# Kernel tuning notes

Measured on AMD Instinct MI355X. Metric: run time of the kernel, lower is better.

## Reference

```python
import jax, jax.numpy as jnp
import numpy as np

B, T, C, H = 4, 2048, 2048, 16
D = C // H  # head dim = 128


def setup_inputs() -> dict:
    key = jax.random.key(0)
    k1, k2, k3, k4 = jax.random.split(key, 4)
    x = jax.random.normal(k1, (B, T, C), dtype=jnp.float32)
    # per-token key mask; force token 0 valid so no causal row is fully masked
    tok_mask = jax.random.randint(k2, (B, T), 0, 2).astype(bool).at[:, 0].set(True)
    s = 1.0 / np.sqrt(C).astype(np.float32)
    W_qkv = jax.random.normal(k3, (C, 3 * C), dtype=jnp.float32) * s
    W_proj = jax.random.normal(k4, (C, C), dtype=jnp.float32) * s
    return {"x": x, "tok_mask": tok_mask, "W_qkv": W_qkv, "W_proj": W_proj}


def reference(x, tok_mask, W_qkv, W_proj):
    Bx, Tx, Cx = x.shape
    qkv = x @ W_qkv                              # [B,T,3C]
    q, k, v = jnp.split(qkv, 3, axis=-1)
    q = q.reshape(Bx, Tx, H, D)
    k = k.reshape(Bx, Tx, H, D)
    v = v.reshape(Bx, Tx, H, D)
    scale = 1.0 / np.sqrt(D).astype(np.float32)
    scores = jnp.einsum('bqhd,bkhd->bhqk', q, k) * scale  # [B,H,T,T]
    causal = jnp.tril(jnp.ones((Tx, Tx), dtype=bool))      # [T,T]
    # tok_mask broadcasts over the query dim (key mask), AND-ed with causal
    mask = tok_mask[:, None, :] & causal                   # [B,T,T]
    scores = jnp.where(mask[:, None, :, :], scores, -jnp.inf)
    attn = jax.nn.softmax(scores, axis=-1)                 # dropout p=0 -> identity
    y = jnp.einsum('bhqk,bkhd->bqhd', attn, v).reshape(Bx, Tx, Cx)
    return y @ W_proj
```

## Files before the change

### kernel.cpp

```cpp
#include <hip/hip_runtime.h>
#include <hip/hip_bf16.h>
#include <stdint.h>

typedef __bf16 bf16;
typedef __bf16 bf16x8 __attribute__((ext_vector_type(8)));
typedef float f32x4 __attribute__((ext_vector_type(4)));
typedef unsigned short u16;
typedef unsigned int u32;

constexpr int NB = 4;
constexpr int NT = 2048;
constexpr int NC = 2048;
constexpr int NH = 16;
constexpr int ND = 128;
constexpr int NC3 = 6144;

__device__ __forceinline__ void gload16(const void* g, void* l) {
  __builtin_amdgcn_global_load_lds((const __attribute__((address_space(1))) void*)g,
                                   (__attribute__((address_space(3))) void*)l, 16, 0, 0);
}

__device__ __forceinline__ u32 pack_bf16(float a, float b) {
  return (u32)__builtin_bit_cast(u16, (bf16)a) | ((u32)__builtin_bit_cast(u16, (bf16)b) << 16);
}

__global__ __launch_bounds__(256) void ingest_k(const float* __restrict__ raw, bf16* __restrict__ out, long n) {
  long i = ((long)blockIdx.x * 256 + threadIdx.x) * 8;
  if (i >= n) return;
  f32x4 a = *(const f32x4*)(raw + i), b = *(const f32x4*)(raw + i + 4);
  bf16x8 o;
  o[0] = (bf16)a[0]; o[1] = (bf16)a[1]; o[2] = (bf16)a[2]; o[3] = (bf16)a[3];
  o[4] = (bf16)b[0]; o[5] = (bf16)b[1]; o[6] = (bf16)b[2]; o[7] = (bf16)b[3];
  *(bf16x8*)(out + i) = o;
}

__global__ void mask_prep_k(const void* raw, int* out) {
  __shared__ int s_gt1, s_oddnz, s_allb, s_allf, s_allh;
  if (threadIdx.x == 0) { s_gt1 = 0; s_oddnz = 0; s_allb = 1; s_allf = 1; s_allh = 1; }
  __syncthreads();
  const unsigned int* mw = (const unsigned int*)raw;
  int gt1 = 0, oddnz = 0, allb = 1, allf = 1, allh = 1;
  for (int i = threadIdx.x; i < 2048; i += 256) {
    unsigned v = mw[i];
    if (v > 1u) gt1 = 1;
    if ((i & 1) && v) oddnz = 1;
#pragma unroll
    for (int bb = 0; bb < 4; ++bb) { unsigned by = (v >> (8*bb)) & 0xffu; if (by > 1u) allb = 0; }
    if (v != 0u && v != 0x3F800000u) allf = 0;
    unsigned lo = v & 0xffffu, hi = v >> 16;
    if ((lo != 0u && lo != 0x3F80u) || (hi != 0u && hi != 0x3F80u)) allh = 0;
  }
  if (gt1) atomicOr(&s_gt1, 1);
  if (oddnz) atomicOr(&s_oddnz, 1);
  if (!allb) atomicAnd(&s_allb, 0);
  if (!allf) atomicAnd(&s_allf, 0);
  if (!allh) atomicAnd(&s_allh, 0);
  __syncthreads();
  int mode;
  if (!s_gt1)       mode = s_oddnz ? 0 : 2;
  else if (s_allf)  mode = 3;
  else if (s_allb)  mode = 1;
  else if (s_allh)  mode = 4;
  else              mode = 0;
  for (int i = threadIdx.x; i < NB*NT; i += 256) {
    int v;
    if (mode == 0)      v = (((const int*)raw)[i] != 0);
    else if (mode == 1) v = (((const unsigned char*)raw)[i] != 0);
    else if (mode == 2) v = (((const long long*)raw)[i] != 0);
    else if (mode == 3) v = (((const unsigned int*)raw)[i] != 0);
    else                v = (((const unsigned short*)raw)[i] != 0);
    out[i] = v;
  }
}

__global__ __launch_bounds__(256) void transpose_f32_k(const float* __restrict__ in, bf16* __restrict__ out,
                                                       int in_rs, int out_rs) {
  __shared__ __align__(16) bf16 t[64][72];
  const int r0 = blockIdx.y << 6, c0 = blockIdx.x << 6;
  const int tid = threadIdx.x;
#pragma unroll
  for (int i = 0; i < 4; ++i) {
    int slot = i*256 + tid, row = slot >> 4, c4 = slot & 15;
    f32x4 v = *(const f32x4*)(in + (long)(r0 + row)*in_rs + c0 + c4*4);
#pragma unroll
    for (int e = 0; e < 4; ++e) t[c4*4 + e][row] = (bf16)v[e];
  }
  __syncthreads();
#pragma unroll
  for (int i = 0; i < 2; ++i) {
    int slot = i*256 + tid, row = slot >> 3, c8 = slot & 7;
    bf16x8 v = *(const bf16x8*)(&t[row][c8*8]);
    *(bf16x8*)(out + (long)(c0 + row)*out_rs + r0 + c8*8) = v;
  }
}

__global__ __launch_bounds__(256) void vtrans_k(const bf16* __restrict__ qkv, bf16* __restrict__ vt) {
  __shared__ __align__(16) bf16 t[64][72];
  const int tt = blockIdx.x, dh = blockIdx.y, bh = blockIdx.z;
  const int b = bh >> 4, h = bh & 15;
  const int tid = threadIdx.x;
  const bf16* src = qkv + (long)(b*NT + tt*64)*NC3 + (2*NC + h*ND + dh*64);
#pragma unroll
  for (int i = 0; i < 2; ++i) {
    int slot = i*256 + tid, row = slot >> 3, c8 = slot & 7;
    bf16x8 v = *(const bf16x8*)(src + (long)row*NC3 + c8*8);
#pragma unroll
    for (int e = 0; e < 8; ++e) t[c8*8 + e][row] = v[e];
  }
  __syncthreads();
  bf16* dst = vt + ((long)bh*ND + dh*64)*NT + tt*64;
#pragma unroll
  for (int i = 0; i < 2; ++i) {
    int slot = i*256 + tid, row = slot >> 3, c8 = slot & 7;
    bf16x8 v = *(const bf16x8*)(&t[row][c8*8]);
    *(bf16x8*)(dst + (long)row*NT + c8*8) = v;
  }
}

template <typename OT>
__global__ __launch_bounds__(512, 2) void gemm256_k(const bf16* __restrict__ A, const bf16* __restrict__ BT,
                                                    OT* __restrict__ Cout, int M, int N, int K, int nbx) {
  const int nwg = gridDim.x;
  const int bid = blockIdx.x;
  const int cpx = nwg >> 3;
  const int swz = (bid & 7) * cpx + (bid >> 3);
  const int bx = swz % nbx, by = swz / nbx;
  const long m0 = (long)by << 8, n0 = (long)bx << 8;

  const int tid = threadIdx.x, w = tid >> 6, l = tid & 63, g = l >> 4, r = l & 15;
  const int wm = w >> 2, wn = w & 3;

  __shared__ __align__(16) char As[2][32768];
  __shared__ __align__(16) char Bs[2][32768];

  long aoff[4], boff[4];
  int slo[4];
#pragma unroll
  for (int i = 0; i < 4; ++i) {
    int s = i*512 + tid, row = s >> 3, c = s & 7, cp = c ^ (row & 7);
    aoff[i] = (m0 + row)*(long)K + cp*8;
    boff[i] = (n0 + row)*(long)K + cp*8;
    slo[i] = (i*512 + w*64) << 4;
  }

  const f32x4 z4 = {0.f, 0.f, 0.f, 0.f};
  f32x4 acc[8][4];
#pragma unroll
  for (int i = 0; i < 8; ++i)
#pragma unroll
    for (int j = 0; j < 4; ++j) acc[i][j] = z4;

  const int nk = K >> 6;
#pragma unroll
  for (int i = 0; i < 4; ++i) {
    gload16(A + aoff[i], As[0] + slo[i]);
    gload16(BT + boff[i], Bs[0] + slo[i]);
  }
  __syncthreads();

  bf16x8 af[8], bfr[4];

  for (int t = 0; t < nk; ++t) {
    const int cur = t & 1;
    const char* Ac = As[cur];
    const char* Bc = Bs[cur];

#pragma unroll
    for (int mi = 0; mi < 4; ++mi)
#pragma unroll
      for (int kk = 0; kk < 2; ++kk) {
        int row = wm*128 + mi*16 + r;
        af[mi*2+kk] = *(const bf16x8*)(Ac + row*128 + (((kk*4 + g) ^ (row & 7)) << 4));
      }
#pragma unroll
    for (int ni = 0; ni < 2; ++ni)
#pragma unroll
      for (int kk = 0; kk < 2; ++kk) {
        int row = wn*64 + ni*16 + r;
        bfr[ni*2+kk] = *(const bf16x8*)(Bc + row*128 + (((kk*4 + g) ^ (row & 7)) << 4));
      }
    if (t + 1 < nk) {
      const long ko = (long)(t+1) << 6;
#pragma unroll
      for (int i = 0; i < 4; ++i) {
        gload16(A + aoff[i] + ko, As[cur^1] + slo[i]);
        gload16(BT + boff[i] + ko, Bs[cur^1] + slo[i]);
      }
    }
    __builtin_amdgcn_s_setprio(1);
#pragma unroll
    for (int mi = 0; mi < 4; ++mi)
#pragma unroll
      for (int ni = 0; ni < 2; ++ni)
#pragma unroll
        for (int kk = 0; kk < 2; ++kk)
          acc[mi][ni] = __builtin_amdgcn_mfma_f32_16x16x32_bf16(af[mi*2+kk], bfr[ni*2+kk], acc[mi][ni], 0, 0, 0);
    __builtin_amdgcn_s_setprio(0);
    __builtin_amdgcn_s_barrier();

#pragma unroll
    for (int mi = 0; mi < 4; ++mi)
#pragma unroll
      for (int kk = 0; kk < 2; ++kk) {
        int row = wm*128 + 64 + mi*16 + r;
        af[mi*2+kk] = *(const bf16x8*)(Ac + row*128 + (((kk*4 + g) ^ (row & 7)) << 4));
      }
    __builtin_amdgcn_s_setprio(1);
#pragma unroll
    for (int mi = 0; mi < 4; ++mi)
#pragma unroll
      for (int ni = 0; ni < 2; ++ni)
#pragma unroll
        for (int kk = 0; kk < 2; ++kk)
          acc[4+mi][ni] = __builtin_amdgcn_mfma_f32_16x16x32_bf16(af[mi*2+kk], bfr[ni*2+kk], acc[4+mi][ni], 0, 0, 0);
    __builtin_amdgcn_s_setprio(0);
    __builtin_amdgcn_s_barrier();

#pragma unroll
    for (int ni = 0; ni < 2; ++ni)
#pragma unroll
      for (int kk = 0; kk < 2; ++kk) {
        int row = wn*64 + 32 + ni*16 + r;
        bfr[ni*2+kk] = *(const bf16x8*)(Bc + row*128 + (((kk*4 + g) ^ (row & 7)) << 4));
      }
    __builtin_amdgcn_s_setprio(1);
#pragma unroll
    for (int mi = 0; mi < 4; ++mi)
#pragma unroll
      for (int ni = 0; ni < 2; ++ni)
#pragma unroll
        for (int kk = 0; kk < 2; ++kk)
          acc[4+mi][2+ni] = __builtin_amdgcn_mfma_f32_16x16x32_bf16(af[mi*2+kk], bfr[ni*2+kk], acc[4+mi][2+ni], 0, 0, 0);
    __builtin_amdgcn_s_setprio(0);
    __builtin_amdgcn_s_barrier();

#pragma unroll
    for (int mi = 0; mi < 4; ++mi)
#pragma unroll
      for (int kk = 0; kk < 2; ++kk) {
        int row = wm*128 + mi*16 + r;
        af[mi*2+kk] = *(const bf16x8*)(Ac + row*128 + (((kk*4 + g) ^ (row & 7)) << 4));
      }
    __builtin_amdgcn_s_setprio(1);
#pragma unroll
    for (int mi = 0; mi < 4; ++mi)
#pragma unroll
      for (int ni = 0; ni < 2; ++ni)
#pragma unroll
        for (int kk = 0; kk < 2; ++kk)
          acc[mi][2+ni] = __builtin_amdgcn_mfma_f32_16x16x32_bf16(af[mi*2+kk], bfr[ni*2+kk], acc[mi][2+ni], 0, 0, 0);
    __builtin_amdgcn_s_setprio(0);
    __syncthreads();
  }

#pragma unroll
  for (int mi = 0; mi < 8; ++mi)
#pragma unroll
    for (int ni = 0; ni < 4; ++ni)
#pragma unroll
      for (int j = 0; j < 4; ++j) {
        long mr = m0 + wm*128 + mi*16 + 4*g + j;
        long nc = n0 + wn*64 + ni*16 + r;
        Cout[mr*(long)N + nc] = (OT)acc[mi][ni][j];
      }
}

__global__ __launch_bounds__(256, 2) void attn_k(const bf16* __restrict__ qkv, const bf16* __restrict__ vt,
                                                 const int* __restrict__ mask, bf16* __restrict__ y) {
  const int qx = blockIdx.x, h = blockIdx.y, b = blockIdx.z;
  const int qt = (qx & 1) ? (31 - (qx >> 1)) : (qx >> 1);
  const int tid = threadIdx.x, w = tid >> 6, l = tid & 63, g = l >> 4, r = l & 15;
  const int q0 = qt << 6;
  const int bh = b*NH + h;
  const int ntiles = qt + 1;
  const int qrow = q0 + w*16 + r;

  __shared__ __align__(16) char Klds[2][16384];
  __shared__ __align__(16) char Vlds[2][16384];
  __shared__ __align__(16) char Plds[8192];
  __shared__ char Mc[2048];
  char* Pl = Plds + (w << 11);

  for (int i = tid; i < q0 + 64; i += 256) Mc[i] = (char)(mask[b*NT + i] != 0);

  long koff[4], voff[4];
  int klo[4];
#pragma unroll
  for (int i = 0; i < 4; ++i) {
    int slot = i*256 + tid;
    int row = slot >> 4, c = slot & 15, cp = c ^ (row & 7);
    koff[i] = (long)row*NC3 + cp*8;
    klo[i] = (i*256 + w*64) << 4;
    int vrow = slot >> 3, vc = slot & 7, vcp = vc ^ (vrow & 7);
    voff[i] = (long)vrow*NT + vcp*8;
  }
  const bf16* kbase0 = qkv + (long)(b*NT)*NC3 + (NC + h*ND);
  const bf16* vbase0 = vt + (long)bh*ND*NT;

  bf16x8 qf[4];
  {
    const bf16* qp = qkv + (long)(b*NT + qrow)*NC3 + h*ND + g*8;
#pragma unroll
    for (int dk = 0; dk < 4; ++dk) qf[dk] = *(const bf16x8*)(qp + dk*32);
  }

  const f32x4 z4 = {0.f, 0.f, 0.f, 0.f};
  f32x4 acc[8];
#pragma unroll
  for (int i = 0; i < 8; ++i) acc[i] = z4;
  float m_run = 0.0f;
  float l_run = 0.0f;

  const float SCL = 0.08838834764831845f * 1.4426950408889634f;

#pragma unroll
  for (int i = 0; i < 4; ++i) {
    gload16(kbase0 + koff[i], Klds[0] + klo[i]);
    gload16(vbase0 + voff[i], Vlds[0] + klo[i]);
  }
  __syncthreads();

  for (int kt = 0; kt < ntiles; ++kt) {
    const int cur = kt & 1;
    if (kt + 1 < ntiles) {
      const bf16* kb = kbase0 + (long)((kt+1)*64)*NC3;
      const bf16* vb = vbase0 + (kt+1)*64;
#pragma unroll
      for (int i = 0; i < 4; ++i) {
        gload16(kb + koff[i], Klds[cur^1] + klo[i]);
        gload16(vb + voff[i], Vlds[cur^1] + klo[i]);
      }
    }
    const char* Kl = Klds[cur];
    const char* Vl = Vlds[cur];
    const int key0 = kt*64;
    const bool act = (key0 <= q0 + w*16 + 15);

    if (act) {
      u32 mw_[4];
#pragma unroll
      for (int kc = 0; kc < 4; ++kc) mw_[kc] = *(const u32*)(Mc + key0 + kc*16 + 4*g);

      float tv[4][4];
      __builtin_amdgcn_s_setprio(1);
#pragma unroll
      for (int kc = 0; kc < 4; ++kc) {
        const int krow = kc*16 + r;
        f32x4 s = z4;
#pragma unroll
        for (int dk = 0; dk < 4; ++dk) {
          bf16x8 kf = *(const bf16x8*)(Kl + krow*256 + (((dk*4 + g) ^ (krow & 7)) << 4));
          s = __builtin_amdgcn_mfma_f32_16x16x32_bf16(kf, qf[dk], s, 0, 0, 0);
        }
#pragma unroll
        for (int j = 0; j < 4; ++j) {
          const int key = key0 + kc*16 + 4*g + j;
          const bool ok = ((mw_[kc] >> (8*j)) & 0xffu) && (key <= qrow);
          tv[kc][j] = ok ? s[j]*SCL : -3.0e38f;
        }
      }
      __builtin_amdgcn_s_setprio(0);

      float tmax = -3.0e38f;
#pragma unroll
      for (int kc = 0; kc < 4; ++kc)
#pragma unroll
        for (int j = 0; j < 4; ++j) tmax = fmaxf(tmax, tv[kc][j]);
      tmax = fmaxf(tmax, __shfl_xor(tmax, 16));
      tmax = fmaxf(tmax, __shfl_xor(tmax, 32));

      if (!__all(tmax <= m_run + 8.0f)) {
        float mn = fmaxf(m_run, tmax);
        float al = exp2f(m_run - mn);
        m_run = mn;
        l_run *= al;
        float alj[4];
#pragma unroll
        for (int j = 0; j < 4; ++j) alj[j] = __shfl(al, 4*g + j);
#pragma unroll
        for (int d0 = 0; d0 < 8; ++d0)
#pragma unroll
          for (int j = 0; j < 4; ++j) acc[d0][j] *= alj[j];
      }

      float rs = 0.f;
      u32 pk0[4], pk1[4];
#pragma unroll
      for (int kc = 0; kc < 4; ++kc) {
        float p0 = exp2f(tv[kc][0] - m_run), p1 = exp2f(tv[kc][1] - m_run);
        float p2 = exp2f(tv[kc][2] - m_run), p3 = exp2f(tv[kc][3] - m_run);
        rs += (p0 + p1) + (p2 + p3);
        pk0[kc] = pack_bf16(p0, p1);
        pk1[kc] = pack_bf16(p2, p3);
      }
      rs += __shfl_xor(rs, 16);
      rs += __shfl_xor(rs, 32);
      l_run += rs;
#pragma unroll
      for (int kc = 0; kc < 4; ++kc) {
        const int off = (kc*32 + g*8) ^ ((r & 7) << 4);
        uint2 wv; wv.x = pk0[kc]; wv.y = pk1[kc];
        *(uint2*)(Pl + r*128 + off) = wv;
      }
      asm volatile("s_waitcnt lgkmcnt(0)" ::: "memory");
      __builtin_amdgcn_sched_barrier(0);
      bf16x8 pa[2];
#pragma unroll
      for (int kk = 0; kk < 2; ++kk)
        pa[kk] = *(const bf16x8*)(Pl + r*128 + ((kk*64 + g*16) ^ ((r & 7) << 4)));

      __builtin_amdgcn_s_setprio(1);
#pragma unroll
      for (int d0 = 0; d0 < 8; ++d0) {
        const int vrow = d0*16 + r;
#pragma unroll
        for (int kk = 0; kk < 2; ++kk) {
          bf16x8 vf = *(const bf16x8*)(Vl + vrow*128 + (((kk*4 + g) ^ (vrow & 7)) << 4));
          acc[d0] = __builtin_amdgcn_mfma_f32_16x16x32_bf16(pa[kk], vf, acc[d0], 0, 0, 0);
        }
      }
      __builtin_amdgcn_s_setprio(0);
    }
    __syncthreads();
  }

  float lr[4];
#pragma unroll
  for (int j = 0; j < 4; ++j) lr[j] = __shfl(l_run, 4*g + j);
#pragma unroll
  for (int d0 = 0; d0 < 8; ++d0)
#pragma unroll
    for (int j = 0; j < 4; ++j) {
      int qr = q0 + w*16 + 4*g + j;
      y[(long)(b*NT + qr)*NC + h*ND + d0*16 + r] = (bf16)(acc[d0][j] / lr[j]);
    }
}

extern "C" void kernel_launch(void* const* d_in, const int* in_sizes, int n_in,
                              void* d_out, int out_size, void* d_ws, size_t ws_size,
                              hipStream_t stream) {
  const float* xr     = (const float*)d_in[0];
  const void*  tok    = d_in[1];
  const float* wqkvr  = (const float*)d_in[2];
  const float* wprojr = (const float*)d_in[3];
  float* out = (float*)d_out;
  char* ws = (char*)d_ws;

  bf16* qkv    = (bf16*)(ws);
  bf16* yattn  = (bf16*)(ws + 100663296L);
  bf16* wT     = (bf16*)(ws + 134217728L);
  bf16* wpT    = (bf16*)(ws + 159383552L);
  bf16* xb     = (bf16*)(ws + 167772160L);
  bf16* vtb    = xb;
  int*  maskI  = (int*)(ws + 201326592L);

  mask_prep_k<<<1, 256, 0, stream>>>(tok, maskI);
  ingest_k<<<8192, 256, 0, stream>>>(xr, xb, 16777216L);
  transpose_f32_k<<<dim3(96, 32), 256, 0, stream>>>(wqkvr, wT, NC3, NC);
  transpose_f32_k<<<dim3(32, 32), 256, 0, stream>>>(wprojr, wpT, NC, NC);
  gemm256_k<bf16><<<768, 512, 0, stream>>>(xb, wT, qkv, 8192, 6144, 2048, 24);
  vtrans_k<<<dim3(32, 2, 64), 256, 0, stream>>>(qkv, vtb);
  attn_k<<<dim3(32, 16, 4), 256, 0, stream>>>(qkv, vtb, maskI, yattn);
  gemm256_k<float><<<256, 512, 0, stream>>>(yattn, wpT, out, 8192, 2048, 2048, 8);
}
```

Baseline: 589.8 us.

## Double query rows per wave in attention to reuse K/V tiles

The attention kernel now processes 128 query rows per block, with each wave handling two 16-row query groups that share the same K and V fragments loaded from LDS. This halves the grid and the K/V global-to-LDS traffic per query row, and amortises LDS fragment reads over twice the MFMA work. In exchange, register pressure roughly doubles (two accumulator sets), so launch bounds drop to one block per SIMD-occupancy target. The coarser causal tiles also add some wasted work on diagonal blocks and reduce load balancing granularity.

```diff
diff --git a/kernel.cpp b/kernel.cpp
--- a/kernel.cpp
+++ b/kernel.cpp
@@ -265,23 +265,25 @@
       }
 }
 
-__global__ __launch_bounds__(256, 2) void attn_k(const bf16* __restrict__ qkv, const bf16* __restrict__ vt,
+__global__ __launch_bounds__(256, 1) void attn_k(const bf16* __restrict__ qkv, const bf16* __restrict__ vt,
                                                  const int* __restrict__ mask, bf16* __restrict__ y) {
   const int qx = blockIdx.x, h = blockIdx.y, b = blockIdx.z;
-  const int qt = (qx & 1) ? (31 - (qx >> 1)) : (qx >> 1);
+  const int qb = (qx & 1) ? (15 - (qx >> 1)) : (qx >> 1);
   const int tid = threadIdx.x, w = tid >> 6, l = tid & 63, g = l >> 4, r = l & 15;
-  const int q0 = qt << 6;
+  const int q0 = qb << 7;
   const int bh = b*NH + h;
-  const int ntiles = qt + 1;
-  const int qrow = q0 + w*16 + r;
+  const int ntiles = (qb << 1) + 2;
+  const int qrowA = q0 + w*32 + r;
+  const int qrowB = qrowA + 16;
 
   __shared__ __align__(16) char Klds[2][16384];
   __shared__ __align__(16) char Vlds[2][16384];
-  __shared__ __align__(16) char Plds[8192];
+  __shared__ __align__(16) char Plds[16384];
   __shared__ char Mc[2048];
-  char* Pl = Plds + (w << 11);
-
-  for (int i = tid; i < q0 + 64; i += 256) Mc[i] = (char)(mask[b*NT + i] != 0);
+  char* PlA = Plds + (w << 12);
+  char* PlB = PlA + 2048;
+
+  for (int i = tid; i < q0 + 128; i += 256) Mc[i] = (char)(mask[b*NT + i] != 0);
 
   long koff[4], voff[4];
   int klo[4];
@@ -297,19 +299,23 @@
   const bf16* kbase0 = qkv + (long)(b*NT)*NC3 + (NC + h*ND);
   const bf16* vbase0 = vt + (long)bh*ND*NT;
 
-  bf16x8 qf[4];
+  bf16x8 qfA[4], qfB[4];
   {
-    const bf16* qp = qkv + (long)(b*NT + qrow)*NC3 + h*ND + g*8;
-#pragma unroll
-    for (int dk = 0; dk < 4; ++dk) qf[dk] = *(const bf16x8*)(qp + dk*32);
+    const bf16* qpA = qkv + (long)(b*NT + qrowA)*NC3 + h*ND + g*8;
+    const bf16* qpB = qkv + (long)(b*NT + qrowB)*NC3 + h*ND + g*8;
+#pragma unroll
+    for (int dk = 0; dk < 4; ++dk) {
+      qfA[dk] = *(const bf16x8*)(qpA + dk*32);
+      qfB[dk] = *(const bf16x8*)(qpB + dk*32);
+    }
   }
 
   const f32x4 z4 = {0.f, 0.f, 0.f, 0.f};
-  f32x4 acc[8];
-#pragma unroll
-  for (int i = 0; i < 8; ++i) acc[i] = z4;
-  float m_run = 0.0f;
-  float l_run = 0.0f;
+  f32x4 accA[8], accB[8];
+#pragma unroll
+  for (int i = 0; i < 8; ++i) { accA[i] = z4; accB[i] = z4; }
+  float m_runA = 0.0f, l_runA = 0.0f;
+  float m_runB = 0.0f, l_runB = 0.0f;
 
   const float SCL = 0.08838834764831845f * 1.4426950408889634f;
 
@@ -334,80 +340,122 @@
     const char* Kl = Klds[cur];
     const char* Vl = Vlds[cur];
     const int key0 = kt*64;
-    const bool act = (key0 <= q0 + w*16 + 15);
-
-    if (act) {
+    const bool actB = (key0 <= q0 + w*32 + 31);
+    const bool actA = (key0 <= q0 + w*32 + 15);
+
+    if (actB) {
       u32 mw_[4];
 #pragma unroll
       for (int kc = 0; kc < 4; ++kc) mw_[kc] = *(const u32*)(Mc + key0 + kc*16 + 4*g);
 
-      float tv[4][4];
+      float tvA[4][4], tvB[4][4];
       __builtin_amdgcn_s_setprio(1);
 #pragma unroll
       for (int kc = 0; kc < 4; ++kc) {
         const int krow = kc*16 + r;
-        f32x4 s = z4;
-#pragma unroll
-        for (int dk = 0; dk < 4; ++dk) {
-          bf16x8 kf = *(const bf16x8*)(Kl + krow*256 + (((dk*4 + g) ^ (krow & 7)) << 4));
-          s = __builtin_amdgcn_mfma_f32_16x16x32_bf16(kf, qf[dk], s, 0, 0, 0);
+        bf16x8 kf[4];
+#pragma unroll
+        for (int dk = 0; dk < 4; ++dk)
+          kf[dk] = *(const bf16x8*)(Kl + krow*256 + (((dk*4 + g) ^ (krow & 7)) << 4));
+        f32x4 sB = z4;
+#pragma unroll
+        for (int dk = 0; dk < 4; ++dk)
+          sB = __builtin_amdgcn_mfma_f32_16x16x32_bf16(kf[dk], qfB[dk], sB, 0, 0, 0);
+        f32x4 sA = z4;
+        if (actA) {
+#pragma unroll
+          for (int dk = 0; dk < 4; ++dk)
+            sA = __builtin_amdgcn_mfma_f32_16x16x32_bf16(kf[dk], qfA[dk], sA, 0, 0, 0);
         }
 #pragma unroll
         for (int j = 0; j < 4; ++j) {
           const int key = key0 + kc*16 + 4*g + j;
-          const bool ok = ((mw_[kc] >> (8*j)) & 0xffu) && (key <= qrow);
-          tv[kc][j] = ok ? s[j]*SCL : -3.0e38f;
+          const bool km = ((mw_[kc] >> (8*j)) & 0xffu) != 0;
+          tvB[kc][j] = (km && key <= qrowB) ? sB[j]*SCL : -3.0e38f;
+          tvA[kc][j] = (km && key <= qrowA) ? sA[j]*SCL : -3.0e38f;
         }
       }
       __builtin_amdgcn_s_setprio(0);
 
-      float tmax = -3.0e38f;
-#pragma unroll
-      for (int kc = 0; kc < 4; ++kc)
-#pragma unroll
-        for (int j = 0; j < 4; ++j) tmax = fmaxf(tmax, tv[kc][j]);
-      tmax = fmaxf(tmax, __shfl_xor(tmax, 16));
-      tmax = fmaxf(tmax, __shfl_xor(tmax, 32));
-
-      if (!__all(tmax <= m_run + 8.0f)) {
-        float mn = fmaxf(m_run, tmax);
-        float al = exp2f(m_run - mn);
-        m_run = mn;
-        l_run *= al;
-        float alj[4];
-#pragma unroll
-        for (int j = 0; j < 4; ++j) alj[j] = __shfl(al, 4*g + j);
-#pragma unroll
-        for (int d0 = 0; d0 < 8; ++d0)
-#pragma unroll
-          for (int j = 0; j < 4; ++j) acc[d0][j] *= alj[j];
-      }
-
-      float rs = 0.f;
-      u32 pk0[4], pk1[4];
-#pragma unroll
-      for (int kc = 0; kc < 4; ++kc) {
-        float p0 = exp2f(tv[kc][0] - m_run), p1 = exp2f(tv[kc][1] - m_run);
-        float p2 = exp2f(tv[kc][2] - m_run), p3 = exp2f(tv[kc][3] - m_run);
-        rs += (p0 + p1) + (p2 + p3);
-        pk0[kc] = pack_bf16(p0, p1);
-        pk1[kc] = pack_bf16(p2, p3);
-      }
-      rs += __shfl_xor(rs, 16);
-      rs += __shfl_xor(rs, 32);
-      l_run += rs;
-#pragma unroll
-      for (int kc = 0; kc < 4; ++kc) {
-        const int off = (kc*32 + g*8) ^ ((r & 7) << 4);
-        uint2 wv; wv.x = pk0[kc]; wv.y = pk1[kc];
-        *(uint2*)(Pl + r*128 + off) = wv;
-      }
+      {
+        float tmax = -3.0e38f;
+#pragma unroll
+        for (int kc = 0; kc < 4; ++kc)
+#pragma unroll
+          for (int j = 0; j < 4; ++j) tmax = fmaxf(tmax, tvB[kc][j]);
+        tmax = fmaxf(tmax, __shfl_xor(tmax, 16));
+        tmax = fmaxf(tmax, __shfl_xor(tmax, 32));
+        if (!__all(tmax <= m_runB + 8.0f)) {
+          float mn = fmaxf(m_runB, tmax);
+          float al = exp2f(m_runB - mn);
+          m_runB = mn;
+          l_runB *= al;
+          float alj[4];
+#pragma unroll
+          for (int j = 0; j < 4; ++j) alj[j] = __shfl(al, 4*g + j);
+#pragma unroll
+          for (int d0 = 0; d0 < 8; ++d0)
+#pragma unroll
+            for (int j = 0; j < 4; ++j) accB[d0][j] *= alj[j];
+        }
+        float rs = 0.f;
+#pragma unroll
+        for (int kc = 0; kc < 4; ++kc) {
+          float p0 = exp2f(tvB[kc][0] - m_runB), p1 = exp2f(tvB[kc][1] - m_runB);
+          float p2 = exp2f(tvB[kc][2] - m_runB), p3 = exp2f(tvB[kc][3] - m_runB);
+          rs += (p0 + p1) + (p2 + p3);
+          const int off = (kc*32 + g*8) ^ ((r & 7) << 4);
+          uint2 wv; wv.x = pack_bf16(p0, p1); wv.y = pack_bf16(p2, p3);
+          *(uint2*)(PlB + r*128 + off) = wv;
+        }
+        rs += __shfl_xor(rs, 16);
+        rs += __shfl_xor(rs, 32);
+        l_runB += rs;
+      }
+      if (actA) {
+        float tmax = -3.0e38f;
+#pragma unroll
+        for (int kc = 0; kc < 4; ++kc)
+#pragma unroll
+          for (int j = 0; j < 4; ++j) tmax = fmaxf(tmax, tvA[kc][j]);
+        tmax = fmaxf(tmax, __shfl_xor(tmax, 16));
+        tmax = fmaxf(tmax, __shfl_xor(tmax, 32));
+        if (!__all(tmax <= m_runA + 8.0f)) {
+          float mn = fmaxf(m_runA, tmax);
+          float al = exp2f(m_runA - mn);
+          m_runA = mn;
+          l_runA *= al;
+          float alj[4];
+#pragma unroll
+          for (int j = 0; j < 4; ++j) alj[j] = __shfl(al, 4*g + j);
+#pragma unroll
+          for (int d0 = 0; d0 < 8; ++d0)
+#pragma unroll
+            for (int j = 0; j < 4; ++j) accA[d0][j] *= alj[j];
+        }
+        float rs = 0.f;
+#pragma unroll
+        for (int kc = 0; kc < 4; ++kc) {
+          float p0 = exp2f(tvA[kc][0] - m_runA), p1 = exp2f(tvA[kc][1] - m_runA);
+          float p2 = exp2f(tvA[kc][2] - m_runA), p3 = exp2f(tvA[kc][3] - m_runA);
+          rs += (p0 + p1) + (p2 + p3);
+          const int off = (kc*32 + g*8) ^ ((r & 7) << 4);
+          uint2 wv; wv.x = pack_bf16(p0, p1); wv.y = pack_bf16(p2, p3);
+          *(uint2*)(PlA + r*128 + off) = wv;
+        }
+        rs += __shfl_xor(rs, 16);
+        rs += __shfl_xor(rs, 32);
+        l_runA += rs;
+      }
+
       asm volatile("s_waitcnt lgkmcnt(0)" ::: "memory");
       __builtin_amdgcn_sched_barrier(0);
-      bf16x8 pa[2];
-#pragma unroll
-      for (int kk = 0; kk < 2; ++kk)
-        pa[kk] = *(const bf16x8*)(Pl + r*128 + ((kk*64 + g*16) ^ ((r & 7) << 4)));
+      bf16x8 paA[2], paB[2];
+#pragma unroll
+      for (int kk = 0; kk < 2; ++kk) {
+        paB[kk] = *(const bf16x8*)(PlB + r*128 + ((kk*64 + g*16) ^ ((r & 7) << 4)));
+        paA[kk] = *(const bf16x8*)(PlA + r*128 + ((kk*64 + g*16) ^ ((r & 7) << 4)));
+      }
 
       __builtin_amdgcn_s_setprio(1);
 #pragma unroll
@@ -416,7 +464,8 @@
 #pragma unroll
         for (int kk = 0; kk < 2; ++kk) {
           bf16x8 vf = *(const bf16x8*)(Vl + vrow*128 + (((kk*4 + g) ^ (vrow & 7)) << 4));
-          acc[d0] = __builtin_amdgcn_mfma_f32_16x16x32_bf16(pa[kk], vf, acc[d0], 0, 0, 0);
+          accB[d0] = __builtin_amdgcn_mfma_f32_16x16x32_bf16(paB[kk], vf, accB[d0], 0, 0, 0);
+          if (actA) accA[d0] = __builtin_amdgcn_mfma_f32_16x16x32_bf16(paA[kk], vf, accA[d0], 0, 0, 0);
         }
       }
       __builtin_amdgcn_s_setprio(0);
@@ -424,16 +473,22 @@
     __syncthreads();
   }
 
-  float lr[4];
-#pragma unroll
-  for (int j = 0; j < 4; ++j) lr[j] = __shfl(l_run, 4*g + j);
-#pragma unroll
-  for (int d0 = 0; d0 < 8; ++d0)
+  {
+    float lrA[4], lrB[4];
 #pragma unroll
     for (int j = 0; j < 4; ++j) {
-      int qr = q0 + w*16 + 4*g + j;
-      y[(long)(b*NT + qr)*NC + h*ND + d0*16 + r] = (bf16)(acc[d0][j] / lr[j]);
+      lrA[j] = __shfl(l_runA, 4*g + j);
+      lrB[j] = __shfl(l_runB, 4*g + j);
     }
+#pragma unroll
+    for (int d0 = 0; d0 < 8; ++d0)
+#pragma unroll
+      for (int j = 0; j < 4; ++j) {
+        int qrA = q0 + w*32 + 4*g + j;
+        y[(long)(b*NT + qrA)*NC + h*ND + d0*16 + r] = (bf16)(accA[d0][j] / lrA[j]);
+        y[(long)(b*NT + qrA + 16)*NC + h*ND + d0*16 + r] = (bf16)(accB[d0][j] / lrB[j]);
+      }
+  }
 }
 
 extern "C" void kernel_launch(void* const* d_in, const int* in_sizes, int n_in,
@@ -460,6 +515,6 @@
   transpose_f32_k<<<dim3(32, 32), 256, 0, stream>>>(wprojr, wpT, NC, NC);
   gemm256_k<bf16><<<768, 512, 0, stream>>>(xb, wT, qkv, 8192, 6144, 2048, 24);
   vtrans_k<<<dim3(32, 2, 64), 256, 0, stream>>>(qkv, vtb);
-  attn_k<<<dim3(32, 16, 4), 256, 0, stream>>>(qkv, vtb, maskI, yattn);
+  attn_k<<<dim3(16, 16, 4), 256, 0, stream>>>(qkv, vtb, maskI, yattn);
   gemm256_k<float><<<256, 512, 0, stream>>>(yattn, wpT, out, 8192, 2048, 2048, 8);
 }
```

Measured after the change: 803.0 us. +36.1%, slower.
